# Performance work log

Measured on AMD Instinct MI355X. Metric: run time of the kernel, lower is better.

The kernel has to match this reference:

```python
import jax, jax.numpy as jnp
import numpy as np

TEMP = 0.5
EPS = 1e-12  # matches torch F.normalize default eps


def _l2_normalize(x):
    n = jnp.sqrt(jnp.sum(x * x, axis=1, keepdims=True))
    return x / jnp.maximum(n, EPS)


def setup_inputs() -> dict:
    key = jax.random.key(0)
    k1, k2 = jax.random.split(key)
    B, D = 4096, 256
    return {
        "x_i": jax.random.normal(k1, (B, D), dtype=jnp.float32),
        "x_j": jax.random.normal(k2, (B, D), dtype=jnp.float32),
    }


def reference(x_i, x_j):
    B = x_i.shape[0]
    z = jnp.concatenate([_l2_normalize(x_i), _l2_normalize(x_j)], axis=0)  # [2B, D]
    # cosine similarity of normalized vectors == plain matmul
    sim = z @ z.T  # [2B, 2B]
    pos = jnp.concatenate([jnp.diagonal(sim, B), jnp.diagonal(sim, -B)], axis=0)  # [2B]
    neg_mask = 1.0 - jnp.eye(2 * B, dtype=sim.dtype)
    denom = jnp.sum(neg_mask * jnp.exp(sim / TEMP), axis=1)  # [2B]
    # -log(exp(pos/T) / denom) = -pos/T + log(denom)
    loss = jnp.sum(-(pos / TEMP) + jnp.log(denom)) / (2 * B)
    return loss
```

## Files before the change

### kernel.cpp

```cpp
#include <hip/hip_runtime.h>
#include <hip/hip_bf16.h>

#define B_ROWS 4096
#define NROWS  8192
#define D      256
#define NPANEL 32
#define NSEG   32
#define NBLK2  512
#define TT     264

typedef __attribute__((ext_vector_type(8))) short bf16x8;
typedef __attribute__((ext_vector_type(4))) float floatx4;

__global__ __launch_bounds__(256) void norm_pos_kernel(
    const float* __restrict__ xi, const float* __restrict__ xj,
    short* __restrict__ z, float* __restrict__ pos,
    float* __restrict__ selfdot, float* __restrict__ rowsum,
    float* __restrict__ out, unsigned int* __restrict__ counter) {
    int gt = blockIdx.x * 256 + threadIdx.x;
    if (gt < NROWS) rowsum[gt] = 0.f;
    if (gt == 0) { out[0] = 0.f; counter[0] = 0u; }

    int p    = blockIdx.x * 4 + (threadIdx.x >> 6);
    int lane = threadIdx.x & 63;
    float4 v1 = ((const float4*)(xi + (size_t)p * D))[lane];
    float4 v2 = ((const float4*)(xj + (size_t)p * D))[lane];
    float ss1 = v1.x * v1.x + v1.y * v1.y + v1.z * v1.z + v1.w * v1.w;
    float ss2 = v2.x * v2.x + v2.y * v2.y + v2.z * v2.z + v2.w * v2.w;
#pragma unroll
    for (int off = 32; off > 0; off >>= 1) {
        ss1 += __shfl_xor(ss1, off);
        ss2 += __shfl_xor(ss2, off);
    }
    float sc1 = 1.0f / fmaxf(sqrtf(ss1), 1e-12f);
    float sc2 = 1.0f / fmaxf(sqrtf(ss2), 1e-12f);

    union { __hip_bfloat16 h[4]; short4 s4; } u1, u2;
    u1.h[0] = __float2bfloat16(v1.x * sc1); u1.h[1] = __float2bfloat16(v1.y * sc1);
    u1.h[2] = __float2bfloat16(v1.z * sc1); u1.h[3] = __float2bfloat16(v1.w * sc1);
    u2.h[0] = __float2bfloat16(v2.x * sc2); u2.h[1] = __float2bfloat16(v2.y * sc2);
    u2.h[2] = __float2bfloat16(v2.z * sc2); u2.h[3] = __float2bfloat16(v2.w * sc2);
    ((short4*)(z + (size_t)p * D))[lane]            = u1.s4;
    ((short4*)(z + (size_t)(p + B_ROWS) * D))[lane] = u2.s4;

    float sd1 = 0.f, sd2 = 0.f, dp = 0.f;
#pragma unroll
    for (int j = 0; j < 4; j++) {
        float a = __bfloat162float(u1.h[j]);
        float b = __bfloat162float(u2.h[j]);
        sd1 += a * a; sd2 += b * b; dp += a * b;
    }
#pragma unroll
    for (int off = 32; off > 0; off >>= 1) {
        sd1 += __shfl_xor(sd1, off);
        sd2 += __shfl_xor(sd2, off);
        dp  += __shfl_xor(dp,  off);
    }
    if (lane == 0) {
        pos[p] = dp; pos[p + B_ROWS] = dp;
        selfdot[p] = sd1; selfdot[p + B_ROWS] = sd2;
    }
}

__global__ __launch_bounds__(256, 2) void sim_rowsum_kernel(
    const short* __restrict__ z, float* __restrict__ rowsum,
    const float* __restrict__ pos, const float* __restrict__ selfdot,
    unsigned int* __restrict__ counter, float* __restrict__ out) {
    __shared__ __align__(16) short Bbuf[2][8192];
    __shared__ unsigned int done_s;
    __shared__ float sdata[4];

    const int tid  = threadIdx.x;
    const int lane = tid & 63;
    const int w    = tid >> 6;
    const int lm   = lane & 15;
    const int lg   = lane >> 4;

    const int s  = blockIdx.x >> 5;
    const int q  = blockIdx.x & 31;
    const int L0 = 256 - 8 * s;
    const int cb = (q * TT) >> 5;
    const int ce = ((q + 1) * TT) >> 5;

    const int scol = tid >> 3;
    const int sg   = tid & 7;
    const int sxor = scol & 7;

    const int fxor = lm & 7;

    bf16x8 a[8][4];
    floatx4 acc[4][2];
    float rsacc[4][4];
    bf16x8 pf[4];

#pragma unroll
    for (int mi = 0; mi < 4; mi++)
#pragma unroll
        for (int r = 0; r < 4; r++) rsacc[mi][r] = 0.f;

    auto decode = [&](int c, int& panel, int& colbase, bool& mirror) {
        int cloc;
        if (c < L0) { panel = s;      cloc = c; }
        else        { panel = 31 - s; cloc = c - L0; }
        colbase = panel * 256 + cloc * 32;
        mirror  = (cloc >= 8);
    };

    auto loadA = [&](int panel) {
#pragma unroll
        for (int kk = 0; kk < 8; kk++)
#pragma unroll
            for (int mi = 0; mi < 4; mi++)
                a[kk][mi] = *(const bf16x8*)(
                    z + (size_t)(panel * 256 + w * 64 + mi * 16 + lm) * D +
                    kk * 32 + lg * 8);
    };

    auto flushRs = [&](int panel) {
#pragma unroll
        for (int mi = 0; mi < 4; mi++)
#pragma unroll
            for (int r = 0; r < 4; r++) {
                float v = rsacc[mi][r];
                v += __shfl_xor(v, 1); v += __shfl_xor(v, 2);
                v += __shfl_xor(v, 4); v += __shfl_xor(v, 8);
                if (lm == 0)
                    atomicAdd(&rowsum[panel * 256 + w * 64 + mi * 16 + lg * 4 + r], v);
                rsacc[mi][r] = 0.f;
            }
    };

    auto fetch = [&](int colbase) {
        const short* p = z + (size_t)(colbase + scol) * D + sg * 8;
#pragma unroll
        for (int j = 0; j < 4; j++) pf[j] = *(const bf16x8*)(p + j * 64);
    };
    auto writeB = [&](int buf) {
#pragma unroll
        for (int j = 0; j < 4; j++) {
            int u = scol * 32 + ((sg + 8 * j) ^ sxor);
            *(bf16x8*)(&Bbuf[buf][u * 8]) = pf[j];
        }
    };

    int panel, colbase; bool mirror;
    decode(cb, panel, colbase, mirror);
    int curpanel = panel;
    fetch(colbase);
    writeB(0);
    loadA(panel);
    __syncthreads();

    for (int c = cb; c < ce; c++) {
        const int buf = (c - cb) & 1;
        decode(c, panel, colbase, mirror);

        const bool hn = (c + 1 < ce);
        if (hn) {
            int npanel, ncolbase; bool nm;
            decode(c + 1, npanel, ncolbase, nm);
            fetch(ncolbase);
        }
        if (panel != curpanel) {
            flushRs(curpanel);
            loadA(panel);
            curpanel = panel;
        }

#pragma unroll
        for (int mi = 0; mi < 4; mi++)
#pragma unroll
            for (int ni = 0; ni < 2; ni++)
                acc[mi][ni] = (floatx4){0.f, 0.f, 0.f, 0.f};

#pragma unroll
        for (int kk = 0; kk < 8; kk++) {
            bf16x8 b0 = *(const bf16x8*)(
                &Bbuf[buf][(( (0 * 16 + lm) * 32) + ((kk * 4 + lg) ^ fxor)) * 8]);
            bf16x8 b1 = *(const bf16x8*)(
                &Bbuf[buf][(( (1 * 16 + lm) * 32) + ((kk * 4 + lg) ^ fxor)) * 8]);
#pragma unroll
            for (int mi = 0; mi < 4; mi++)
                acc[mi][0] = __builtin_amdgcn_mfma_f32_16x16x32_bf16(
                    a[kk][mi], b0, acc[mi][0], 0, 0, 0);
#pragma unroll
            for (int mi = 0; mi < 4; mi++)
                acc[mi][1] = __builtin_amdgcn_mfma_f32_16x16x32_bf16(
                    a[kk][mi], b1, acc[mi][1], 0, 0, 0);
        }

        float cs0 = 0.f, cs1 = 0.f;
#pragma unroll
        for (int mi = 0; mi < 4; mi++)
#pragma unroll
            for (int r = 0; r < 4; r++) {
                float e0 = __expf(2.0f * acc[mi][0][r]);
                float e1 = __expf(2.0f * acc[mi][1][r]);
                rsacc[mi][r] += e0 + e1;
                cs0 += e0; cs1 += e1;
            }
        if (mirror) {
            cs0 += __shfl_xor(cs0, 16); cs0 += __shfl_xor(cs0, 32);
            cs1 += __shfl_xor(cs1, 16); cs1 += __shfl_xor(cs1, 32);
            if (lane < 16) {
                atomicAdd(&rowsum[colbase + lane],      cs0);
                atomicAdd(&rowsum[colbase + 16 + lane], cs1);
            }
        }

        if (hn) {
            writeB(buf ^ 1);
            __syncthreads();
        }
    }
    flushRs(curpanel);

    __syncthreads();
    if (tid == 0) {
        __threadfence();
        done_s = atomicAdd(counter, 1u);
    }
    __syncthreads();
    if (done_s == (unsigned int)(NBLK2 - 1)) {
        __threadfence();
        float acc_l = 0.f;
#pragma unroll 4
        for (int r = tid; r < NROWS; r += 256) {
            float rsv = __hip_atomic_load(&rowsum[r], __ATOMIC_RELAXED,
                                          __HIP_MEMORY_SCOPE_AGENT);
            float denom = rsv - __expf(2.0f * selfdot[r]);
            acc_l += -2.0f * pos[r] + logf(denom);
        }
#pragma unroll
        for (int off = 32; off > 0; off >>= 1) acc_l += __shfl_xor(acc_l, off);
        if (lane == 0) sdata[w] = acc_l;
        __syncthreads();
        if (tid == 0)
            out[0] = (sdata[0] + sdata[1] + sdata[2] + sdata[3]) / (float)NROWS;
    }
}

extern "C" void kernel_launch(void* const* d_in, const int* in_sizes, int n_in,
                              void* d_out, int out_size, void* d_ws, size_t ws_size,
                              hipStream_t stream) {
    const float* xi = (const float*)d_in[0];
    const float* xj = (const float*)d_in[1];
    float* out      = (float*)d_out;

    char* ws        = (char*)d_ws;
    short* z        = (short*)ws;
    float* rowsum   = (float*)(ws + (size_t)NROWS * D * 2);
    float* pos      = rowsum + NROWS;
    float* selfdot  = pos + NROWS;
    unsigned int* counter = (unsigned int*)(selfdot + NROWS);

    norm_pos_kernel<<<B_ROWS / 4, 256, 0, stream>>>(xi, xj, z, pos, selfdot,
                                                    rowsum, out, counter);
    sim_rowsum_kernel<<<NBLK2, 256, 0, stream>>>(z, rowsum, pos, selfdot,
                                                 counter, out);
}
```

Measured before the change: 99.84 us.

## Switch similarity GEMM to FP8 MFMA with in-kernel diagonal masking and more blocks

Normalized rows are quantized to FP8 (e4m3) instead of bf16, and the similarity tile loop now uses the 16x16x32 fp8 MFMA. That halves the z footprint and the LDS/global traffic, and the shared tile shrinks so three blocks can fit per CU. The self-similarity term is now masked directly inside diagonal tiles instead of being subtracted afterwards, which removes the selfdot buffer. The column segmentation grows from 32 to 48 segments, giving 768 blocks. The risk is lower precision in the loss, since FP8 dot products feed exp(2*sim).

After: 109.7 us. 1.1x slower.

```diff
diff --git a/kernel.cpp b/kernel.cpp
--- a/kernel.cpp
+++ b/kernel.cpp
@@ -4,19 +4,17 @@
 #define B_ROWS 4096
 #define NROWS  8192
 #define D      256
-#define NPANEL 32
-#define NSEG   32
-#define NBLK2  512
+#define NSEG   48
+#define NBLK2  768
 #define TT     264
 
-typedef __attribute__((ext_vector_type(8))) short bf16x8;
 typedef __attribute__((ext_vector_type(4))) float floatx4;
 
 __global__ __launch_bounds__(256) void norm_pos_kernel(
     const float* __restrict__ xi, const float* __restrict__ xj,
-    short* __restrict__ z, float* __restrict__ pos,
-    float* __restrict__ selfdot, float* __restrict__ rowsum,
-    float* __restrict__ out, unsigned int* __restrict__ counter) {
+    unsigned char* __restrict__ z, float* __restrict__ pos,
+    float* __restrict__ rowsum, float* __restrict__ out,
+    unsigned int* __restrict__ counter) {
     int gt = blockIdx.x * 256 + threadIdx.x;
     if (gt < NROWS) rowsum[gt] = 0.f;
     if (gt == 0) { out[0] = 0.f; counter[0] = 0u; }
@@ -35,38 +33,27 @@
     float sc1 = 1.0f / fmaxf(sqrtf(ss1), 1e-12f);
     float sc2 = 1.0f / fmaxf(sqrtf(ss2), 1e-12f);
 
-    union { __hip_bfloat16 h[4]; short4 s4; } u1, u2;
-    u1.h[0] = __float2bfloat16(v1.x * sc1); u1.h[1] = __float2bfloat16(v1.y * sc1);
-    u1.h[2] = __float2bfloat16(v1.z * sc1); u1.h[3] = __float2bfloat16(v1.w * sc1);
-    u2.h[0] = __float2bfloat16(v2.x * sc2); u2.h[1] = __float2bfloat16(v2.y * sc2);
-    u2.h[2] = __float2bfloat16(v2.z * sc2); u2.h[3] = __float2bfloat16(v2.w * sc2);
-    ((short4*)(z + (size_t)p * D))[lane]            = u1.s4;
-    ((short4*)(z + (size_t)(p + B_ROWS) * D))[lane] = u2.s4;
-
-    float sd1 = 0.f, sd2 = 0.f, dp = 0.f;
-#pragma unroll
-    for (int j = 0; j < 4; j++) {
-        float a = __bfloat162float(u1.h[j]);
-        float b = __bfloat162float(u2.h[j]);
-        sd1 += a * a; sd2 += b * b; dp += a * b;
-    }
-#pragma unroll
-    for (int off = 32; off > 0; off >>= 1) {
-        sd1 += __shfl_xor(sd1, off);
-        sd2 += __shfl_xor(sd2, off);
-        dp  += __shfl_xor(dp,  off);
-    }
-    if (lane == 0) {
-        pos[p] = dp; pos[p + B_ROWS] = dp;
-        selfdot[p] = sd1; selfdot[p + B_ROWS] = sd2;
-    }
+    float n1x = v1.x * sc1, n1y = v1.y * sc1, n1z = v1.z * sc1, n1w = v1.w * sc1;
+    float n2x = v2.x * sc2, n2y = v2.y * sc2, n2z = v2.z * sc2, n2w = v2.w * sc2;
+
+    float dp = n1x * n2x + n1y * n2y + n1z * n2z + n1w * n2w;
+#pragma unroll
+    for (int off = 32; off > 0; off >>= 1) dp += __shfl_xor(dp, off);
+    if (lane == 0) { pos[p] = dp; pos[p + B_ROWS] = dp; }
+
+    int q1 = __builtin_amdgcn_cvt_pk_fp8_f32(n1x, n1y, 0, false);
+    q1     = __builtin_amdgcn_cvt_pk_fp8_f32(n1z, n1w, q1, true);
+    int q2 = __builtin_amdgcn_cvt_pk_fp8_f32(n2x, n2y, 0, false);
+    q2     = __builtin_amdgcn_cvt_pk_fp8_f32(n2z, n2w, q2, true);
+    ((int*)(z + (size_t)p * D))[lane]            = q1;
+    ((int*)(z + (size_t)(p + B_ROWS) * D))[lane] = q2;
 }
 
-__global__ __launch_bounds__(256, 2) void sim_rowsum_kernel(
-    const short* __restrict__ z, float* __restrict__ rowsum,
-    const float* __restrict__ pos, const float* __restrict__ selfdot,
-    unsigned int* __restrict__ counter, float* __restrict__ out) {
-    __shared__ __align__(16) short Bbuf[2][8192];
+__global__ __launch_bounds__(256, 3) void sim_rowsum_kernel(
+    const unsigned char* __restrict__ z, float* __restrict__ rowsum,
+    const float* __restrict__ pos, unsigned int* __restrict__ counter,
+    float* __restrict__ out) {
+    __shared__ __align__(16) int4 Bbuf[2][512];
     __shared__ unsigned int done_s;
     __shared__ float sdata[4];
 
@@ -76,34 +63,32 @@
     const int lm   = lane & 15;
     const int lg   = lane >> 4;
 
-    const int s  = blockIdx.x >> 5;
-    const int q  = blockIdx.x & 31;
+    const int s  = blockIdx.x / NSEG;
+    const int q  = blockIdx.x % NSEG;
     const int L0 = 256 - 8 * s;
-    const int cb = (q * TT) >> 5;
-    const int ce = ((q + 1) * TT) >> 5;
-
-    const int scol = tid >> 3;
-    const int sg   = tid & 7;
-    const int sxor = scol & 7;
-
-    const int fxor = lm & 7;
-
-    bf16x8 a[8][4];
+    const int cb = (q * TT) / NSEG;
+    const int ce = ((q + 1) * TT) / NSEG;
+
+    const int scol = tid & 31;
+    const int ssg  = tid >> 5;
+
+    const int crow = lg >> 1;
+    const int half = (lg & 1) * 8;
+
+    long long a[8][4];
     floatx4 acc[4][2];
     float rsacc[4][4];
-    bf16x8 pf[4];
+    int4 pf0, pf1;
 
 #pragma unroll
     for (int mi = 0; mi < 4; mi++)
 #pragma unroll
         for (int r = 0; r < 4; r++) rsacc[mi][r] = 0.f;
 
-    auto decode = [&](int c, int& panel, int& colbase, bool& mirror) {
-        int cloc;
+    auto decode = [&](int c, int& panel, int& colbase, int& cloc) {
         if (c < L0) { panel = s;      cloc = c; }
         else        { panel = 31 - s; cloc = c - L0; }
         colbase = panel * 256 + cloc * 32;
-        mirror  = (cloc >= 8);
     };
 
     auto loadA = [&](int panel) {
@@ -111,7 +96,7 @@
         for (int kk = 0; kk < 8; kk++)
 #pragma unroll
             for (int mi = 0; mi < 4; mi++)
-                a[kk][mi] = *(const bf16x8*)(
+                a[kk][mi] = *(const long long*)(
                     z + (size_t)(panel * 256 + w * 64 + mi * 16 + lm) * D +
                     kk * 32 + lg * 8);
     };
@@ -131,20 +116,17 @@
     };
 
     auto fetch = [&](int colbase) {
-        const short* p = z + (size_t)(colbase + scol) * D + sg * 8;
-#pragma unroll
-        for (int j = 0; j < 4; j++) pf[j] = *(const bf16x8*)(p + j * 64);
+        const unsigned char* p = z + (size_t)(colbase + scol) * D + ssg * 32;
+        pf0 = *(const int4*)p;
+        pf1 = *(const int4*)(p + 16);
     };
     auto writeB = [&](int buf) {
-#pragma unroll
-        for (int j = 0; j < 4; j++) {
-            int u = scol * 32 + ((sg + 8 * j) ^ sxor);
-            *(bf16x8*)(&Bbuf[buf][u * 8]) = pf[j];
-        }
-    };
-
-    int panel, colbase; bool mirror;
-    decode(cb, panel, colbase, mirror);
+        Bbuf[buf][(ssg * 2 + 0) * 32 + scol] = pf0;
+        Bbuf[buf][(ssg * 2 + 1) * 32 + scol] = pf1;
+    };
+
+    int panel, colbase, cloc;
+    decode(cb, panel, colbase, cloc);
     int curpanel = panel;
     fetch(colbase);
     writeB(0);
@@ -153,12 +135,12 @@
 
     for (int c = cb; c < ce; c++) {
         const int buf = (c - cb) & 1;
-        decode(c, panel, colbase, mirror);
+        decode(c, panel, colbase, cloc);
 
         const bool hn = (c + 1 < ce);
         if (hn) {
-            int npanel, ncolbase; bool nm;
-            decode(c + 1, npanel, ncolbase, nm);
+            int npanel, ncolbase, ncloc;
+            decode(c + 1, npanel, ncolbase, ncloc);
             fetch(ncolbase);
         }
         if (panel != curpanel) {
@@ -173,33 +155,47 @@
             for (int ni = 0; ni < 2; ni++)
                 acc[mi][ni] = (floatx4){0.f, 0.f, 0.f, 0.f};
 
+        const char* bbase = (const char*)Bbuf[buf];
 #pragma unroll
         for (int kk = 0; kk < 8; kk++) {
-            bf16x8 b0 = *(const bf16x8*)(
-                &Bbuf[buf][(( (0 * 16 + lm) * 32) + ((kk * 4 + lg) ^ fxor)) * 8]);
-            bf16x8 b1 = *(const bf16x8*)(
-                &Bbuf[buf][(( (1 * 16 + lm) * 32) + ((kk * 4 + lg) ^ fxor)) * 8]);
-#pragma unroll
-            for (int mi = 0; mi < 4; mi++)
-                acc[mi][0] = __builtin_amdgcn_mfma_f32_16x16x32_bf16(
+            long long b0 = *(const long long*)(
+                bbase + (((kk * 2 + crow) * 32 + lm) * 16) + half);
+            long long b1 = *(const long long*)(
+                bbase + (((kk * 2 + crow) * 32 + 16 + lm) * 16) + half);
+#pragma unroll
+            for (int mi = 0; mi < 4; mi++)
+                acc[mi][0] = __builtin_amdgcn_mfma_f32_16x16x32_fp8_fp8(
                     a[kk][mi], b0, acc[mi][0], 0, 0, 0);
 #pragma unroll
             for (int mi = 0; mi < 4; mi++)
-                acc[mi][1] = __builtin_amdgcn_mfma_f32_16x16x32_bf16(
+                acc[mi][1] = __builtin_amdgcn_mfma_f32_16x16x32_fp8_fp8(
                     a[kk][mi], b1, acc[mi][1], 0, 0, 0);
         }
 
+        const bool diagreg = (cloc < 8);
         float cs0 = 0.f, cs1 = 0.f;
-#pragma unroll
-        for (int mi = 0; mi < 4; mi++)
-#pragma unroll
-            for (int r = 0; r < 4; r++) {
-                float e0 = __expf(2.0f * acc[mi][0][r]);
-                float e1 = __expf(2.0f * acc[mi][1][r]);
-                rsacc[mi][r] += e0 + e1;
-                cs0 += e0; cs1 += e1;
-            }
-        if (mirror) {
+        if (diagreg) {
+            const int rowb = panel * 256 + w * 64 + lg * 4;
+            const int col0 = colbase + lm, col1 = colbase + 16 + lm;
+#pragma unroll
+            for (int mi = 0; mi < 4; mi++)
+#pragma unroll
+                for (int r = 0; r < 4; r++) {
+                    int grow = rowb + mi * 16 + r;
+                    float e0 = (grow == col0) ? 0.f : __expf(2.0f * acc[mi][0][r]);
+                    float e1 = (grow == col1) ? 0.f : __expf(2.0f * acc[mi][1][r]);
+                    rsacc[mi][r] += e0 + e1;
+                }
+        } else {
+#pragma unroll
+            for (int mi = 0; mi < 4; mi++)
+#pragma unroll
+                for (int r = 0; r < 4; r++) {
+                    float e0 = __expf(2.0f * acc[mi][0][r]);
+                    float e1 = __expf(2.0f * acc[mi][1][r]);
+                    rsacc[mi][r] += e0 + e1;
+                    cs0 += e0; cs1 += e1;
+                }
             cs0 += __shfl_xor(cs0, 16); cs0 += __shfl_xor(cs0, 32);
             cs1 += __shfl_xor(cs1, 16); cs1 += __shfl_xor(cs1, 32);
             if (lane < 16) {
@@ -228,8 +224,7 @@
         for (int r = tid; r < NROWS; r += 256) {
             float rsv = __hip_atomic_load(&rowsum[r], __ATOMIC_RELAXED,
                                           __HIP_MEMORY_SCOPE_AGENT);
-            float denom = rsv - __expf(2.0f * selfdot[r]);
-            acc_l += -2.0f * pos[r] + logf(denom);
+            acc_l += -2.0f * pos[r] + logf(rsv);
         }
 #pragma unroll
         for (int off = 32; off > 0; off >>= 1) acc_l += __shfl_xor(acc_l, off);
@@ -248,14 +243,12 @@
     float* out      = (float*)d_out;
 
     char* ws        = (char*)d_ws;
-    short* z        = (short*)ws;
-    float* rowsum   = (float*)(ws + (size_t)NROWS * D * 2);
+    unsigned char* z = (unsigned char*)ws;
+    float* rowsum   = (float*)(ws + (size_t)NROWS * D);
     float* pos      = rowsum + NROWS;
-    float* selfdot  = pos + NROWS;
-    unsigned int* counter = (unsigned int*)(selfdot + NROWS);
-
-    norm_pos_kernel<<<B_ROWS / 4, 256, 0, stream>>>(xi, xj, z, pos, selfdot,
+    unsigned int* counter = (unsigned int*)(pos + NROWS);
+
+    norm_pos_kernel<<<B_ROWS / 4, 256, 0, stream>>>(xi, xj, z, pos,
                                                     rowsum, out, counter);
-    sim_rowsum_kernel<<<NBLK2, 256, 0, stream>>>(z, rowsum, pos, selfdot,
-                                                 counter, out);
+    sim_rowsum_kernel<<<NBLK2, 256, 0, stream>>>(z, rowsum, pos, counter, out);
 }
```
